# Kernel tuning notes

Measured on AMD Instinct MI355X. Metric: run time of the kernel, lower is better.

The kernel has to match this reference:

```python
import jax, jax.numpy as jnp
import numpy as np

N_HEAD = 8
LN_EPS = 1e-5


def _layernorm(x, w, b):
    mu = jnp.mean(x, axis=-1, keepdims=True)
    var = jnp.var(x, axis=-1, keepdims=True)
    return (x - mu) * jax.lax.rsqrt(var + LN_EPS) * w + b


def setup_inputs() -> dict:
    key = jax.random.key(0)
    ks = jax.random.split(key, 8)
    B, T, D, L, V, F = 4, 768, 512, 6, 50304, 2048
    s = 0.02
    return {
        "idx": jax.random.randint(ks[0], (B, T), 0, V),
        "wte": jax.random.normal(ks[1], (V, D), jnp.float32) * s,
        "wpe": jax.random.normal(ks[2], (T, D), jnp.float32) * s,
        "c_attn_w": jax.random.normal(ks[3], (L, 3 * D, D), jnp.float32) * s,
        "c_attn_b": jnp.zeros((L, 3 * D), jnp.float32),
        "c_proj_w": jax.random.normal(ks[4], (L, D, D), jnp.float32) * s,
        "c_proj_b": jnp.zeros((L, D), jnp.float32),
        "fc_w": jax.random.normal(ks[5], (L, F, D), jnp.float32) * s,
        "fc_b": jnp.zeros((L, F), jnp.float32),
        "fc2_w": jax.random.normal(ks[6], (L, D, F), jnp.float32) * s,
        "fc2_b": jnp.zeros((L, D), jnp.float32),
        "ln1_w": jnp.ones((L, D), jnp.float32),
        "ln1_b": jnp.zeros((L, D), jnp.float32),
        "ln2_w": jnp.ones((L, D), jnp.float32),
        "ln2_b": jnp.zeros((L, D), jnp.float32),
        "lnf_w": jnp.ones((D,), jnp.float32),
        "lnf_b": jnp.zeros((D,), jnp.float32),
    }


def _forward(idx, wte, wpe, c_attn_w, c_attn_b, c_proj_w, c_proj_b,
             fc_w, fc_b, fc2_w, fc2_b, ln1_w, ln1_b, ln2_w, ln2_b,
             lnf_w, lnf_b):
    B, T = idx.shape
    D = wte.shape[1]
    hd = D // N_HEAD
    causal = jnp.tril(jnp.ones((T, T), bool))  # [T,T]

    x = wte[idx] + wpe[:T]  # [B,T,D]; dropout is identity in eval

    def block(x, p):
        (aw, ab, pw, pb, fw, fb, f2w, f2b, l1w, l1b, l2w, l2b) = p
        # --- causal self-attention ---
        qkv = x @ aw.T + ab  # [B,T,3D]
        q, k, v = jnp.split(qkv, 3, axis=-1)
        q = q.reshape(B, T, N_HEAD, hd)
        k = k.reshape(B, T, N_HEAD, hd)
        v = v.reshape(B, T, N_HEAD, hd)
        att = jnp.einsum('bqhd,bkhd->bhqk', q, k) * (1.0 / np.sqrt(hd))
        att = jnp.where(causal, att, -jnp.inf)
        att = jax.nn.softmax(att, axis=-1)
        y = jnp.einsum('bhqk,bkhd->bqhd', att, v).reshape(B, T, D)
        y = y @ pw.T + pb
        x = _layernorm(x + y, l1w, l1b)  # post-norm as in source
        # --- feed-forward ---
        h = jax.nn.relu(x @ fw.T + fb)
        h = h @ f2w.T + f2b
        x = _layernorm(x + h, l2w, l2b)
        return x, None

    params = (c_attn_w, c_attn_b, c_proj_w, c_proj_b, fc_w, fc_b,
              fc2_w, fc2_b, ln1_w, ln1_b, ln2_w, ln2_b)
    x, _ = jax.lax.scan(block, x, params)
    x = _layernorm(x, lnf_w, lnf_b)
    logits = x @ wte.T  # tied head, no bias
    return logits


def reference(idx, wte, wpe, c_attn_w, c_attn_b, c_proj_w, c_proj_b,
              fc_w, fc_b, fc2_w, fc2_b, ln1_w, ln1_b, ln2_w, ln2_b,
              lnf_w, lnf_b):
    return _forward(idx, wte, wpe, c_attn_w, c_attn_b, c_proj_w, c_proj_b,
                    fc_w, fc_b, fc2_w, fc2_b, ln1_w, ln1_b, ln2_w, ln2_b,
                    lnf_w, lnf_b)
```

## Files before the change

### kernel.cpp

```cpp
#include <hip/hip_runtime.h>
#include <hip/hip_bf16.h>

#define AS1 __attribute__((address_space(1)))
#define AS3 __attribute__((address_space(3)))

typedef __attribute__((ext_vector_type(8))) short short8;
typedef __attribute__((ext_vector_type(4))) float f32x4;

constexpr int BB = 4, TT = 768, DDIM = 512, LL = 6, VV = 50304, FF = 2048;
constexpr int MM = BB * TT;

__device__ inline unsigned short f2b(float f) {
  union { float f; unsigned u; } a; a.f = f;
  unsigned u = a.u;
  return (unsigned short)((u + 0x7FFFu + ((u >> 16) & 1u)) >> 16);
}
__device__ inline float b2f(unsigned short u) {
  union { unsigned u; float f; } a; a.u = ((unsigned)u) << 16; return a.f;
}

constexpr size_t CW0 = (size_t)VV * DDIM;
constexpr size_t CW1 = CW0 + (size_t)LL * 3 * DDIM * DDIM;
constexpr size_t CW2 = CW1 + (size_t)LL * DDIM * DDIM;
constexpr size_t CW3 = CW2 + (size_t)LL * FF * DDIM;
constexpr size_t CW4 = CW3 + (size_t)LL * DDIM * FF;

__global__ void cvt_all(const float* __restrict__ wte, const float* __restrict__ aw,
                        const float* __restrict__ pw, const float* __restrict__ fw,
                        const float* __restrict__ f2w, ushort* __restrict__ out) {
  size_t i = ((size_t)blockIdx.x * 256 + threadIdx.x) * 4;
  if (i >= CW4) return;
  const float* src; size_t base;
  if (i < CW0)      { src = wte; base = 0; }
  else if (i < CW1) { src = aw;  base = CW0; }
  else if (i < CW2) { src = pw;  base = CW1; }
  else if (i < CW3) { src = fw;  base = CW2; }
  else              { src = f2w; base = CW3; }
  float4 v = *(const float4*)(src + (i - base));
  ushort4 o = { f2b(v.x), f2b(v.y), f2b(v.z), f2b(v.w) };
  *(ushort4*)(out + i) = o;
}

__global__ void embed_kernel(const int* __restrict__ idx, const float* __restrict__ wte,
                             const float* __restrict__ wpe, float* __restrict__ x,
                             ushort* __restrict__ xb) {
  int row = blockIdx.x;
  int t = row % TT;
  int tok = idx[row];
  int c = threadIdx.x * 4;
  float4 a = *(const float4*)(wte + (size_t)tok * DDIM + c);
  float4 p = *(const float4*)(wpe + (size_t)t * DDIM + c);
  a.x += p.x; a.y += p.y; a.z += p.z; a.w += p.w;
  *(float4*)(x + (size_t)row * DDIM + c) = a;
  ushort4 o = { f2b(a.x), f2b(a.y), f2b(a.z), f2b(a.w) };
  *(ushort4*)(xb + (size_t)row * DDIM + c) = o;
}

template <int RELU, int OUTBF16, int BM, int BN, int SPLITK>
__global__ __launch_bounds__(256) void gemm_bt64(
    const ushort* __restrict__ A, const ushort* __restrict__ Bw,
    const float* __restrict__ bias, void* __restrict__ Cv, int Ndim, int K) {
  constexpr int MI = BM / 32, NJ = BN / 32;
  __shared__ ushort sA[2][BM * 64];
  __shared__ ushort sB[2][BN * 64];
  const int tid = threadIdx.x;
  const int wid = tid >> 6, lane = tid & 63;
  const int m0 = blockIdx.y * BM, n0 = blockIdx.x * BN;
  const int kchunk = K / SPLITK;
  const int ks0 = (SPLITK > 1) ? blockIdx.z * kchunk : 0;
  const int wm = (wid >> 1) * (BM / 2), wn = (wid & 1) * (BN / 2);

  f32x4 zero = {0.f, 0.f, 0.f, 0.f};
  f32x4 acc[MI][NJ];
#pragma unroll
  for (int i = 0; i < MI; i++)
#pragma unroll
    for (int j = 0; j < NJ; j++) acc[i][j] = zero;

  const int r = tid >> 3;
  const int cg = ((tid & 7) ^ (r & 7)) * 8;
  const ushort* gA = A + (size_t)(m0 + r) * K + ks0 + cg;
  const ushort* gB = Bw + (size_t)(n0 + r) * K + ks0 + cg;

  auto stage = [&](int buf, int kk) {
    const ushort* a0 = gA + kk * 64;
    const ushort* b0 = gB + kk * 64;
    ushort* dA = &sA[buf][0] + wid * 512;
    ushort* dB = &sB[buf][0] + wid * 512;
#pragma unroll
    for (int p = 0; p < BM / 32; p++)
      __builtin_amdgcn_global_load_lds((const AS1 void*)(a0 + (size_t)p * 32 * K),
                                       (AS3 void*)(dA + p * 2048), 16, 0, 0);
#pragma unroll
    for (int p = 0; p < BN / 32; p++)
      __builtin_amdgcn_global_load_lds((const AS1 void*)(b0 + (size_t)p * 32 * K),
                                       (AS3 void*)(dB + p * 2048), 16, 0, 0);
  };

  const int fr = lane & 15;
  const int fk = (lane >> 4) * 8;
  auto ldfrag = [&](const ushort* s, int rowbase, int sub) -> short8 {
    const int row = rowbase + fr;
    const int off = row * 128 + ((sub * 64 + fk * 2) ^ ((fr & 7) << 4));
    return *(const short8*)((const char*)s + off);
  };

  const int nK = kchunk >> 6;
  stage(0, 0);
  __syncthreads();
  int buf = 0;
  for (int kk = 0; kk < nK; ++kk) {
    if (kk + 1 < nK) stage(buf ^ 1, kk + 1);
    short8 af[MI][2], bf[NJ][2];
#pragma unroll
    for (int i = 0; i < MI; i++)
#pragma unroll
      for (int s = 0; s < 2; s++) af[i][s] = ldfrag(&sA[buf][0], wm + i * 16, s);
#pragma unroll
    for (int j = 0; j < NJ; j++)
#pragma unroll
      for (int s = 0; s < 2; s++) bf[j][s] = ldfrag(&sB[buf][0], wn + j * 16, s);
#pragma unroll
    for (int i = 0; i < MI; i++)
#pragma unroll
      for (int j = 0; j < NJ; j++)
#pragma unroll
        for (int s = 0; s < 2; s++)
          acc[i][j] = __builtin_amdgcn_mfma_f32_16x16x32_bf16(af[i][s], bf[j][s], acc[i][j], 0, 0, 0);
    __syncthreads();
    buf ^= 1;
  }

  const int cr = (lane >> 4) * 4;
  const int cc = lane & 15;
  const size_t zoff = (SPLITK > 1) ? (size_t)blockIdx.z * MM * Ndim : 0;
  ushort* Cb = (ushort*)Cv + zoff;
  float*  Cf = (float*)Cv + zoff;
#pragma unroll
  for (int j = 0; j < NJ; j++) {
    const int gcol = n0 + wn + j * 16 + cc;
    const float bv = (bias && (SPLITK == 1 || blockIdx.z == 0)) ? bias[gcol] : 0.0f;
#pragma unroll
    for (int i = 0; i < MI; i++) {
      const int grow = m0 + wm + i * 16 + cr;
#pragma unroll
      for (int rr = 0; rr < 4; ++rr) {
        float v = acc[i][j][rr] + bv;
        if (RELU) v = fmaxf(v, 0.0f);
        if (OUTBF16)
          Cb[(size_t)(grow + rr) * Ndim + gcol] = f2b(v);
        else
          Cf[(size_t)(grow + rr) * Ndim + gcol] = v;
      }
    }
  }
}

__global__ __launch_bounds__(256) void gemm_head(
    const ushort* __restrict__ A, const ushort* __restrict__ Bw,
    float* __restrict__ Cv, int Ndim, int K) {
  __shared__ ushort sA[2][128 * 32];
  __shared__ ushort sB[2][128 * 32];
  const int tid = threadIdx.x;
  const int wid = tid >> 6, lane = tid & 63;
  int id = blockIdx.x;
  int v = (id >> 3) + (id & 7) * ((int)gridDim.x >> 3);
  const int m0 = (v % 24) * 128;
  const int n0 = (v / 24) * 128;
  const int wm = (wid >> 1) * 64, wn = (wid & 1) * 64;

  f32x4 zero = {0.f, 0.f, 0.f, 0.f};
  f32x4 acc[4][4];
#pragma unroll
  for (int i = 0; i < 4; i++)
#pragma unroll
    for (int j = 0; j < 4; j++) acc[i][j] = zero;

  const int r4 = tid >> 2;
  const int c8 = (tid & 3) * 8;
  const ushort* gA = A + (size_t)(m0 + r4) * K + c8;
  const ushort* gB = Bw + (size_t)(n0 + r4) * K + c8;
  const size_t K64 = (size_t)64 * K;

  auto stage = [&](int buf, int kk) {
    const ushort* a0 = gA + kk * 32;
    const ushort* b0 = gB + kk * 32;
    ushort* dA = &sA[buf][0] + wid * 512;
    ushort* dB = &sB[buf][0] + wid * 512;
#pragma unroll
    for (int i = 0; i < 2; i++)
      __builtin_amdgcn_global_load_lds((const AS1 void*)(a0 + (size_t)i * K64),
                                       (AS3 void*)(dA + i * 2048), 16, 0, 0);
#pragma unroll
    for (int i = 0; i < 2; i++)
      __builtin_amdgcn_global_load_lds((const AS1 void*)(b0 + (size_t)i * K64),
                                       (AS3 void*)(dB + i * 2048), 16, 0, 0);
  };

  const int fr = lane & 15;
  const int fk = (lane >> 4) * 8;
  const int nK = K >> 5;
  stage(0, 0);
  __syncthreads();
  int buf = 0;
  for (int kk = 0; kk < nK; ++kk) {
    if (kk + 1 < nK) stage(buf ^ 1, kk + 1);
    const ushort* pa0 = &sA[buf][0] + (wm + fr) * 32 + fk;
    const ushort* pb0 = &sB[buf][0] + (wn + fr) * 32 + fk;
    short8 af[4], bf[4];
#pragma unroll
    for (int i = 0; i < 4; i++) af[i] = *(const short8*)(pa0 + i * 16 * 32);
#pragma unroll
    for (int j = 0; j < 4; j++) bf[j] = *(const short8*)(pb0 + j * 16 * 32);
#pragma unroll
    for (int i = 0; i < 4; i++)
#pragma unroll
      for (int j = 0; j < 4; j++)
        acc[i][j] = __builtin_amdgcn_mfma_f32_16x16x32_bf16(af[i], bf[j], acc[i][j], 0, 0, 0);
    __syncthreads();
    buf ^= 1;
  }

  const int cr = (lane >> 4) * 4;
  const int cc = lane & 15;
#pragma unroll
  for (int j = 0; j < 4; j++) {
    const int gcol = n0 + wn + j * 16 + cc;
#pragma unroll
    for (int i = 0; i < 4; i++) {
      const int grow = m0 + wm + i * 16 + cr;
#pragma unroll
      for (int rr = 0; rr < 4; ++rr)
        Cv[(size_t)(grow + rr) * Ndim + gcol] = acc[i][j][rr];
    }
  }
}

__device__ inline short8 lds_swz_read(const ushort* base, int row, int elem) {
  return *(const short8*)((const char*)base + row * 128 + ((elem * 2) ^ ((row & 7) << 4)));
}

__global__ __launch_bounds__(256) void attn_mfma(const ushort* __restrict__ qkv,
                                                 ushort* __restrict__ yb) {
  __shared__ ushort sK[64 * 64];
  __shared__ ushort sVT[64 * 64];
  __shared__ ushort sP[4 * 16 * 64];
  const int tid = threadIdx.x;
  const int wid = tid >> 6, lane = tid & 63;
  const int qt = blockIdx.x;
  const int b = blockIdx.y >> 3, h = blockIdx.y & 7;
  const int q0 = qt * 64;
  const int qw = q0 + wid * 16;

  const int fr = lane & 15;
  const int fk = (lane >> 4) * 8;
  ushort* sPw = sP + wid * 16 * 64;

  short8 qf[2];
  {
    const ushort* qp = qkv + (size_t)(b * TT + qw + fr) * 1536 + h * 64;
    qf[0] = *(const short8*)(qp + fk);
    qf[1] = *(const short8*)(qp + 32 + fk);
  }

  const int r4 = tid >> 2;
  const int c32 = (tid & 3) * 16;

  f32x4 zero = {0.f, 0.f, 0.f, 0.f};
  f32x4 acc[4] = {zero, zero, zero, zero};
  float mrow[4] = {-INFINITY, -INFINITY, -INFINITY, -INFINITY};
  float lrow[4] = {0.f, 0.f, 0.f, 0.f};

  for (int kt = 0; kt <= qt; ++kt) {
    __syncthreads();
    const int k0 = kt * 64;
    {
      const ushort* kp = qkv + (size_t)(b * TT + k0 + r4) * 1536 + 512 + h * 64 + c32;
      short8 kv0 = *(const short8*)kp;
      short8 kv1 = *(const short8*)(kp + 8);
      char* skb = (char*)sK + r4 * 128;
      *(short8*)(skb + ((c32 * 2) ^ ((r4 & 7) << 4))) = kv0;
      *(short8*)(skb + ((c32 * 2 + 16) ^ ((r4 & 7) << 4))) = kv1;
      const ushort* vp = kp + 512;
      short8 vv0 = *(const short8*)vp;
      short8 vv1 = *(const short8*)(vp + 8);
#pragma unroll
      for (int i = 0; i < 8; i++) {
        int d0 = c32 + i, d1 = c32 + 8 + i;
        *(ushort*)((char*)sVT + d0 * 128 + ((r4 * 2) ^ ((d0 & 7) << 4))) = (ushort)vv0[i];
        *(ushort*)((char*)sVT + d1 * 128 + ((r4 * 2) ^ ((d1 & 7) << 4))) = (ushort)vv1[i];
      }
    }
    __syncthreads();

    f32x4 sfr[4];
#pragma unroll
    for (int j = 0; j < 4; j++) {
      short8 kb0 = lds_swz_read(sK, j * 16 + fr, fk);
      short8 kb1 = lds_swz_read(sK, j * 16 + fr, 32 + fk);
      f32x4 s = __builtin_amdgcn_mfma_f32_16x16x32_bf16(qf[0], kb0, zero, 0, 0, 0);
      s = __builtin_amdgcn_mfma_f32_16x16x32_bf16(qf[1], kb1, s, 0, 0, 0);
      sfr[j] = s * 0.125f;
    }
    if (kt == qt) {
#pragma unroll
      for (int j = 0; j < 4; j++)
#pragma unroll
        for (int rr = 0; rr < 4; ++rr)
          if (j * 16 + fr > wid * 16 + (lane >> 4) * 4 + rr) sfr[j][rr] = -INFINITY;
    }

    float scl[4];
#pragma unroll
    for (int rr = 0; rr < 4; ++rr) {
      float t = fmaxf(fmaxf(sfr[0][rr], sfr[1][rr]), fmaxf(sfr[2][rr], sfr[3][rr]));
      t = fmaxf(t, __shfl_xor(t, 1));
      t = fmaxf(t, __shfl_xor(t, 2));
      t = fmaxf(t, __shfl_xor(t, 4));
      t = fmaxf(t, __shfl_xor(t, 8));
      const float mnew = fmaxf(mrow[rr], t);
      scl[rr] = __expf(mrow[rr] - mnew);
      mrow[rr] = mnew;
      float ps = 0.f;
#pragma unroll
      for (int j = 0; j < 4; j++) {
        float p = __expf(sfr[j][rr] - mnew);
        sfr[j][rr] = p;
        ps += p;
      }
      ps += __shfl_xor(ps, 1);
      ps += __shfl_xor(ps, 2);
      ps += __shfl_xor(ps, 4);
      ps += __shfl_xor(ps, 8);
      lrow[rr] = lrow[rr] * scl[rr] + ps;
    }

#pragma unroll
    for (int j = 0; j < 4; j++)
#pragma unroll
      for (int rr = 0; rr < 4; ++rr) {
        int q = (lane >> 4) * 4 + rr, k = j * 16 + fr;
        *(ushort*)((char*)sPw + q * 128 + ((k * 2) ^ ((q & 7) << 4))) = f2b(sfr[j][rr]);
      }

#pragma unroll
    for (int f = 0; f < 4; f++)
#pragma unroll
      for (int rr = 0; rr < 4; ++rr) acc[f][rr] *= scl[rr];

    short8 pa0 = lds_swz_read(sPw, fr, fk);
    short8 pa1 = lds_swz_read(sPw, fr, 32 + fk);
#pragma unroll
    for (int f = 0; f < 4; f++) {
      short8 vb0 = lds_swz_read(sVT, f * 16 + fr, fk);
      short8 vb1 = lds_swz_read(sVT, f * 16 + fr, 32 + fk);
      acc[f] = __builtin_amdgcn_mfma_f32_16x16x32_bf16(pa0, vb0, acc[f], 0, 0, 0);
      acc[f] = __builtin_amdgcn_mfma_f32_16x16x32_bf16(pa1, vb1, acc[f], 0, 0, 0);
    }
  }

#pragma unroll
  for (int rr = 0; rr < 4; ++rr) {
    const float inv = 1.0f / lrow[rr];
    const int token = b * TT + qw + (lane >> 4) * 4 + rr;
    ushort* yp = yb + (size_t)token * DDIM + h * 64 + fr;
#pragma unroll
    for (int f = 0; f < 4; f++) yp[f * 16] = f2b(acc[f][rr] * inv);
  }
}

template <int S>
__global__ __launch_bounds__(256) void add_ln(const float* __restrict__ x,
                                              const ushort* __restrict__ y,
                                              const float* __restrict__ w,
                                              const float* __restrict__ bb,
                                              float* __restrict__ xo,
                                              ushort* __restrict__ xb) {
  const int row = blockIdx.x * 4 + (threadIdx.x >> 6);
  const int lane = threadIdx.x & 63;
  const size_t base = (size_t)row * DDIM + lane * 8;
  f32x4 a0 = *(const f32x4*)(x + base);
  f32x4 a1 = *(const f32x4*)(x + base + 4);
#pragma unroll
  for (int s = 0; s < S; ++s) {
    short8 v = *(const short8*)(y + (size_t)s * MM * DDIM + base);
    f32x4 p0 = { b2f((unsigned short)v[0]), b2f((unsigned short)v[1]),
                 b2f((unsigned short)v[2]), b2f((unsigned short)v[3]) };
    f32x4 p1 = { b2f((unsigned short)v[4]), b2f((unsigned short)v[5]),
                 b2f((unsigned short)v[6]), b2f((unsigned short)v[7]) };
    a0 += p0; a1 += p1;
  }
  float sm = (a0[0] + a0[1] + a0[2] + a0[3]) + (a1[0] + a1[1] + a1[2] + a1[3]);
  f32x4 q0 = a0 * a0, q1 = a1 * a1;
  float ss = (q0[0] + q0[1] + q0[2] + q0[3]) + (q1[0] + q1[1] + q1[2] + q1[3]);
#pragma unroll
  for (int o = 1; o < 64; o <<= 1) {
    sm += __shfl_xor(sm, o);
    ss += __shfl_xor(ss, o);
  }
  const float mu = sm * (1.0f / DDIM);
  const float var = ss * (1.0f / DDIM) - mu * mu;
  const float rs = rsqrtf(var + 1e-5f);
  const int c = lane * 8;
  f32x4 w0 = *(const f32x4*)(w + c), w1 = *(const f32x4*)(w + c + 4);
  f32x4 b0 = *(const f32x4*)(bb + c), b1 = *(const f32x4*)(bb + c + 4);
  f32x4 o0 = (a0 - mu) * rs * w0 + b0;
  f32x4 o1 = (a1 - mu) * rs * w1 + b1;
  *(f32x4*)(xo + base) = o0;
  *(f32x4*)(xo + base + 4) = o1;
  ushort4 u0 = { f2b(o0[0]), f2b(o0[1]), f2b(o0[2]), f2b(o0[3]) };
  ushort4 u1 = { f2b(o1[0]), f2b(o1[1]), f2b(o1[2]), f2b(o1[3]) };
  *(ushort4*)(xb + base) = u0;
  *(ushort4*)(xb + base + 4) = u1;
}

extern "C" void kernel_launch(void* const* d_in, const int* in_sizes, int n_in,
                              void* d_out, int out_size, void* d_ws, size_t ws_size,
                              hipStream_t stream) {
  const int*   idx  = (const int*)d_in[0];
  const float* wte  = (const float*)d_in[1];
  const float* wpe  = (const float*)d_in[2];
  const float* aw   = (const float*)d_in[3];
  const float* ab   = (const float*)d_in[4];
  const float* pw   = (const float*)d_in[5];
  const float* pb   = (const float*)d_in[6];
  const float* fw   = (const float*)d_in[7];
  const float* fb   = (const float*)d_in[8];
  const float* f2w  = (const float*)d_in[9];
  const float* f2bi = (const float*)d_in[10];
  const float* l1w  = (const float*)d_in[11];
  const float* l1b  = (const float*)d_in[12];
  const float* l2w  = (const float*)d_in[13];
  const float* l2b  = (const float*)d_in[14];
  const float* lnfw = (const float*)d_in[15];
  const float* lnfb = (const float*)d_in[16];

  char* ws = (char*)d_ws;
  size_t off = 0;
  auto take = [&](size_t bytes) -> void* {
    void* p = ws + off;
    off += (bytes + 255) & ~(size_t)255;
    return p;
  };
  ushort* wte_b = (ushort*)take((size_t)VV * DDIM * 2);
  ushort* aw_b  = (ushort*)take((size_t)LL * 3 * DDIM * DDIM * 2);
  ushort* pw_b  = (ushort*)take((size_t)LL * DDIM * DDIM * 2);
  ushort* fw_b  = (ushort*)take((size_t)LL * FF * DDIM * 2);
  ushort* f2w_b = (ushort*)take((size_t)LL * DDIM * FF * 2);
  float*  x     = (float*)take((size_t)MM * DDIM * 4);
  ushort* xb    = (ushort*)take((size_t)MM * DDIM * 2);
  ushort* qkv_b = (ushort*)take((size_t)MM * 3 * DDIM * 2);
  ushort* yb    = (ushort*)take((size_t)MM * DDIM * 2);
  ushort* tmp_b = (ushort*)take((size_t)2 * MM * DDIM * 2);
  ushort* hb    = (ushort*)take((size_t)MM * FF * 2);

  cvt_all<<<dim3((unsigned)(CW4 / 4 / 256)), dim3(256), 0, stream>>>(
      wte, aw, pw, fw, f2w, wte_b);

  embed_kernel<<<dim3(MM), dim3(128), 0, stream>>>(idx, wte, wpe, x, xb);

  for (int l = 0; l < LL; ++l) {
    gemm_bt64<0, 1, 128, 64, 1><<<dim3(24, 24), dim3(256), 0, stream>>>(
        xb, aw_b + (size_t)l * 3 * DDIM * DDIM, ab + (size_t)l * 3 * DDIM, qkv_b, 3 * DDIM, DDIM);
    attn_mfma<<<dim3(TT / 64, BB * 8), dim3(256), 0, stream>>>(qkv_b, yb);
    gemm_bt64<0, 1, 64, 64, 2><<<dim3(8, 48, 2), dim3(256), 0, stream>>>(
        yb, pw_b + (size_t)l * DDIM * DDIM, pb + (size_t)l * DDIM, tmp_b, DDIM, DDIM);
    add_ln<2><<<dim3(MM / 4), dim3(256), 0, stream>>>(
        x, tmp_b, l1w + (size_t)l * DDIM, l1b + (size_t)l * DDIM, x, xb);
    gemm_bt64<1, 1, 128, 64, 1><<<dim3(32, 24), dim3(256), 0, stream>>>(
        xb, fw_b + (size_t)l * FF * DDIM, fb + (size_t)l * FF, hb, FF, DDIM);
    gemm_bt64<0, 1, 64, 64, 2><<<dim3(8, 48, 2), dim3(256), 0, stream>>>(
        hb, f2w_b + (size_t)l * DDIM * FF, f2bi + (size_t)l * DDIM, tmp_b, DDIM, FF);
    add_ln<2><<<dim3(MM / 4), dim3(256), 0, stream>>>(
        x, tmp_b, l2w + (size_t)l * DDIM, l2b + (size_t)l * DDIM, x, xb);
  }
  add_ln<0><<<dim3(MM / 4), dim3(256), 0, stream>>>(x, nullptr, lnfw, lnfb, x, xb);

  gemm_head<<<dim3((VV / 128) * 24), dim3(256), 0, stream>>>(
      xb, wte_b, (float*)d_out, VV, DDIM);
}
```

Measured before the change: 856.6 us.

## Generalize head GEMM for QKV/FC, vectorize V transpose, keep residual in bf16

The QKV and FC GEMMs now use the 128x128 head-GEMM kernel (K-step 32, bias and ReLU epilogue) in place of the 128x64 tile kernel, which halves the block count and raises reuse per tile. The V transpose into shared memory in attention now loads four rows of 4-wide vectors and writes ushort4 columns instead of scalar 2-byte stores. The fp32 residual stream is removed, so the embedding and the add+layernorm kernels read and write only bf16. This cuts memory traffic but lowers the precision of the residual path.

```diff
diff --git a/kernel.cpp b/kernel.cpp
--- a/kernel.cpp
+++ b/kernel.cpp
@@ -42,8 +42,7 @@
 }
 
 __global__ void embed_kernel(const int* __restrict__ idx, const float* __restrict__ wte,
-                             const float* __restrict__ wpe, float* __restrict__ x,
-                             ushort* __restrict__ xb) {
+                             const float* __restrict__ wpe, ushort* __restrict__ xb) {
   int row = blockIdx.x;
   int t = row % TT;
   int tok = idx[row];
@@ -51,122 +50,29 @@
   float4 a = *(const float4*)(wte + (size_t)tok * DDIM + c);
   float4 p = *(const float4*)(wpe + (size_t)t * DDIM + c);
   a.x += p.x; a.y += p.y; a.z += p.z; a.w += p.w;
-  *(float4*)(x + (size_t)row * DDIM + c) = a;
   ushort4 o = { f2b(a.x), f2b(a.y), f2b(a.z), f2b(a.w) };
   *(ushort4*)(xb + (size_t)row * DDIM + c) = o;
 }
 
-template <int RELU, int OUTBF16, int BM, int BN, int SPLITK>
-__global__ __launch_bounds__(256) void gemm_bt64(
+template <int RELU, int OUTBF16, int BIAS, int SWZ>
+__global__ __launch_bounds__(256) void gemm97(
     const ushort* __restrict__ A, const ushort* __restrict__ Bw,
     const float* __restrict__ bias, void* __restrict__ Cv, int Ndim, int K) {
-  constexpr int MI = BM / 32, NJ = BN / 32;
-  __shared__ ushort sA[2][BM * 64];
-  __shared__ ushort sB[2][BN * 64];
-  const int tid = threadIdx.x;
-  const int wid = tid >> 6, lane = tid & 63;
-  const int m0 = blockIdx.y * BM, n0 = blockIdx.x * BN;
-  const int kchunk = K / SPLITK;
-  const int ks0 = (SPLITK > 1) ? blockIdx.z * kchunk : 0;
-  const int wm = (wid >> 1) * (BM / 2), wn = (wid & 1) * (BN / 2);
-
-  f32x4 zero = {0.f, 0.f, 0.f, 0.f};
-  f32x4 acc[MI][NJ];
-#pragma unroll
-  for (int i = 0; i < MI; i++)
-#pragma unroll
-    for (int j = 0; j < NJ; j++) acc[i][j] = zero;
-
-  const int r = tid >> 3;
-  const int cg = ((tid & 7) ^ (r & 7)) * 8;
-  const ushort* gA = A + (size_t)(m0 + r) * K + ks0 + cg;
-  const ushort* gB = Bw + (size_t)(n0 + r) * K + ks0 + cg;
-
-  auto stage = [&](int buf, int kk) {
-    const ushort* a0 = gA + kk * 64;
-    const ushort* b0 = gB + kk * 64;
-    ushort* dA = &sA[buf][0] + wid * 512;
-    ushort* dB = &sB[buf][0] + wid * 512;
-#pragma unroll
-    for (int p = 0; p < BM / 32; p++)
-      __builtin_amdgcn_global_load_lds((const AS1 void*)(a0 + (size_t)p * 32 * K),
-                                       (AS3 void*)(dA + p * 2048), 16, 0, 0);
-#pragma unroll
-    for (int p = 0; p < BN / 32; p++)
-      __builtin_amdgcn_global_load_lds((const AS1 void*)(b0 + (size_t)p * 32 * K),
-                                       (AS3 void*)(dB + p * 2048), 16, 0, 0);
-  };
-
-  const int fr = lane & 15;
-  const int fk = (lane >> 4) * 8;
-  auto ldfrag = [&](const ushort* s, int rowbase, int sub) -> short8 {
-    const int row = rowbase + fr;
-    const int off = row * 128 + ((sub * 64 + fk * 2) ^ ((fr & 7) << 4));
-    return *(const short8*)((const char*)s + off);
-  };
-
-  const int nK = kchunk >> 6;
-  stage(0, 0);
-  __syncthreads();
-  int buf = 0;
-  for (int kk = 0; kk < nK; ++kk) {
-    if (kk + 1 < nK) stage(buf ^ 1, kk + 1);
-    short8 af[MI][2], bf[NJ][2];
-#pragma unroll
-    for (int i = 0; i < MI; i++)
-#pragma unroll
-      for (int s = 0; s < 2; s++) af[i][s] = ldfrag(&sA[buf][0], wm + i * 16, s);
-#pragma unroll
-    for (int j = 0; j < NJ; j++)
-#pragma unroll
-      for (int s = 0; s < 2; s++) bf[j][s] = ldfrag(&sB[buf][0], wn + j * 16, s);
-#pragma unroll
-    for (int i = 0; i < MI; i++)
-#pragma unroll
-      for (int j = 0; j < NJ; j++)
-#pragma unroll
-        for (int s = 0; s < 2; s++)
-          acc[i][j] = __builtin_amdgcn_mfma_f32_16x16x32_bf16(af[i][s], bf[j][s], acc[i][j], 0, 0, 0);
-    __syncthreads();
-    buf ^= 1;
-  }
-
-  const int cr = (lane >> 4) * 4;
-  const int cc = lane & 15;
-  const size_t zoff = (SPLITK > 1) ? (size_t)blockIdx.z * MM * Ndim : 0;
-  ushort* Cb = (ushort*)Cv + zoff;
-  float*  Cf = (float*)Cv + zoff;
-#pragma unroll
-  for (int j = 0; j < NJ; j++) {
-    const int gcol = n0 + wn + j * 16 + cc;
-    const float bv = (bias && (SPLITK == 1 || blockIdx.z == 0)) ? bias[gcol] : 0.0f;
-#pragma unroll
-    for (int i = 0; i < MI; i++) {
-      const int grow = m0 + wm + i * 16 + cr;
-#pragma unroll
-      for (int rr = 0; rr < 4; ++rr) {
-        float v = acc[i][j][rr] + bv;
-        if (RELU) v = fmaxf(v, 0.0f);
-        if (OUTBF16)
-          Cb[(size_t)(grow + rr) * Ndim + gcol] = f2b(v);
-        else
-          Cf[(size_t)(grow + rr) * Ndim + gcol] = v;
-      }
-    }
-  }
-}
-
-__global__ __launch_bounds__(256) void gemm_head(
-    const ushort* __restrict__ A, const ushort* __restrict__ Bw,
-    float* __restrict__ Cv, int Ndim, int K) {
   __shared__ ushort sA[2][128 * 32];
   __shared__ ushort sB[2][128 * 32];
   const int tid = threadIdx.x;
   const int wid = tid >> 6, lane = tid & 63;
-  int id = blockIdx.x;
-  int v = (id >> 3) + (id & 7) * ((int)gridDim.x >> 3);
-  const int m0 = (v % 24) * 128;
-  const int n0 = (v / 24) * 128;
+  int m0, n0;
+  if (SWZ) {
+    constexpr int MT = MM / 128;
+    int id = blockIdx.x;
+    int v = (id >> 3) + (id & 7) * ((int)gridDim.x >> 3);
+    m0 = (v % MT) * 128;
+    n0 = (v / MT) * 128;
+  } else {
+    m0 = blockIdx.y * 128;
+    n0 = blockIdx.x * 128;
+  }
   const int wm = (wid >> 1) * 64, wn = (wid & 1) * 64;
 
   f32x4 zero = {0.f, 0.f, 0.f, 0.f};
@@ -226,12 +132,112 @@
 #pragma unroll
   for (int j = 0; j < 4; j++) {
     const int gcol = n0 + wn + j * 16 + cc;
+    const float bv = BIAS ? bias[gcol] : 0.0f;
 #pragma unroll
     for (int i = 0; i < 4; i++) {
       const int grow = m0 + wm + i * 16 + cr;
 #pragma unroll
+      for (int rr = 0; rr < 4; ++rr) {
+        float v = acc[i][j][rr] + bv;
+        if (RELU) v = fmaxf(v, 0.0f);
+        if (OUTBF16)
+          ((ushort*)Cv)[(size_t)(grow + rr) * Ndim + gcol] = f2b(v);
+        else
+          ((float*)Cv)[(size_t)(grow + rr) * Ndim + gcol] = v;
+      }
+    }
+  }
+}
+
+template <int SPLITK>
+__global__ __launch_bounds__(256) void gemm_bt64(
+    const ushort* __restrict__ A, const ushort* __restrict__ Bw,
+    const float* __restrict__ bias, ushort* __restrict__ Cv, int Ndim, int K) {
+  constexpr int BM = 64, BN = 64;
+  constexpr int MI = 2, NJ = 2;
+  __shared__ ushort sA[2][BM * 64];
+  __shared__ ushort sB[2][BN * 64];
+  const int tid = threadIdx.x;
+  const int wid = tid >> 6, lane = tid & 63;
+  const int m0 = blockIdx.y * BM, n0 = blockIdx.x * BN;
+  const int kchunk = K / SPLITK;
+  const int ks0 = blockIdx.z * kchunk;
+  const int wm = (wid >> 1) * 32, wn = (wid & 1) * 32;
+
+  f32x4 zero = {0.f, 0.f, 0.f, 0.f};
+  f32x4 acc[MI][NJ];
+#pragma unroll
+  for (int i = 0; i < MI; i++)
+#pragma unroll
+    for (int j = 0; j < NJ; j++) acc[i][j] = zero;
+
+  const int r = tid >> 3;
+  const int cg = ((tid & 7) ^ (r & 7)) * 8;
+  const ushort* gA = A + (size_t)(m0 + r) * K + ks0 + cg;
+  const ushort* gB = Bw + (size_t)(n0 + r) * K + ks0 + cg;
+
+  auto stage = [&](int buf, int kk) {
+    const ushort* a0 = gA + kk * 64;
+    const ushort* b0 = gB + kk * 64;
+    ushort* dA = &sA[buf][0] + wid * 512;
+    ushort* dB = &sB[buf][0] + wid * 512;
+#pragma unroll
+    for (int p = 0; p < 2; p++)
+      __builtin_amdgcn_global_load_lds((const AS1 void*)(a0 + (size_t)p * 32 * K),
+                                       (AS3 void*)(dA + p * 2048), 16, 0, 0);
+#pragma unroll
+    for (int p = 0; p < 2; p++)
+      __builtin_amdgcn_global_load_lds((const AS1 void*)(b0 + (size_t)p * 32 * K),
+                                       (AS3 void*)(dB + p * 2048), 16, 0, 0);
+  };
+
+  const int fr = lane & 15;
+  const int fk = (lane >> 4) * 8;
+  auto ldfrag = [&](const ushort* s, int rowbase, int sub) -> short8 {
+    const int row = rowbase + fr;
+    const int off = row * 128 + ((sub * 64 + fk * 2) ^ ((fr & 7) << 4));
+    return *(const short8*)((const char*)s + off);
+  };
+
+  const int nK = kchunk >> 6;
+  stage(0, 0);
+  __syncthreads();
+  int buf = 0;
+  for (int kk = 0; kk < nK; ++kk) {
+    if (kk + 1 < nK) stage(buf ^ 1, kk + 1);
+    short8 af[MI][2], bf[NJ][2];
+#pragma unroll
+    for (int i = 0; i < MI; i++)
+#pragma unroll
+      for (int s = 0; s < 2; s++) af[i][s] = ldfrag(&sA[buf][0], wm + i * 16, s);
+#pragma unroll
+    for (int j = 0; j < NJ; j++)
+#pragma unroll
+      for (int s = 0; s < 2; s++) bf[j][s] = ldfrag(&sB[buf][0], wn + j * 16, s);
+#pragma unroll
+    for (int i = 0; i < MI; i++)
+#pragma unroll
+      for (int j = 0; j < NJ; j++)
+#pragma unroll
+        for (int s = 0; s < 2; s++)
+          acc[i][j] = __builtin_amdgcn_mfma_f32_16x16x32_bf16(af[i][s], bf[j][s], acc[i][j], 0, 0, 0);
+    __syncthreads();
+    buf ^= 1;
+  }
+
+  const int cr = (lane >> 4) * 4;
+  const int cc = lane & 15;
+  ushort* Cb = Cv + (size_t)blockIdx.z * MM * Ndim;
+#pragma unroll
+  for (int j = 0; j < NJ; j++) {
+    const int gcol = n0 + wn + j * 16 + cc;
+    const float bv = (blockIdx.z == 0) ? bias[gcol] : 0.0f;
+#pragma unroll
+    for (int i = 0; i < MI; i++) {
+      const int grow = m0 + wm + i * 16 + cr;
+#pragma unroll
       for (int rr = 0; rr < 4; ++rr)
-        Cv[(size_t)(grow + rr) * Ndim + gcol] = acc[i][j][rr];
+        Cb[(size_t)(grow + rr) * Ndim + gcol] = f2b(acc[i][j][rr] + bv);
     }
   }
 }
@@ -265,6 +271,8 @@
 
   const int r4 = tid >> 2;
   const int c32 = (tid & 3) * 16;
+  const int kb = (tid >> 4) * 4;
+  const int db = (tid & 15) * 4;
 
   f32x4 zero = {0.f, 0.f, 0.f, 0.f};
   f32x4 acc[4] = {zero, zero, zero, zero};
@@ -281,15 +289,19 @@
       char* skb = (char*)sK + r4 * 128;
       *(short8*)(skb + ((c32 * 2) ^ ((r4 & 7) << 4))) = kv0;
       *(short8*)(skb + ((c32 * 2 + 16) ^ ((r4 & 7) << 4))) = kv1;
-      const ushort* vp = kp + 512;
-      short8 vv0 = *(const short8*)vp;
-      short8 vv1 = *(const short8*)(vp + 8);
-#pragma unroll
-      for (int i = 0; i < 8; i++) {
-        int d0 = c32 + i, d1 = c32 + 8 + i;
-        *(ushort*)((char*)sVT + d0 * 128 + ((r4 * 2) ^ ((d0 & 7) << 4))) = (ushort)vv0[i];
-        *(ushort*)((char*)sVT + d1 * 128 + ((r4 * 2) ^ ((d1 & 7) << 4))) = (ushort)vv1[i];
-      }
+      const ushort* vp = qkv + (size_t)(b * TT + k0 + kb) * 1536 + 1024 + h * 64 + db;
+      ushort4 L0 = *(const ushort4*)vp;
+      ushort4 L1 = *(const ushort4*)(vp + 1536);
+      ushort4 L2 = *(const ushort4*)(vp + 3072);
+      ushort4 L3 = *(const ushort4*)(vp + 4608);
+      ushort4 c0 = { L0.x, L1.x, L2.x, L3.x };
+      ushort4 c1 = { L0.y, L1.y, L2.y, L3.y };
+      ushort4 c2 = { L0.z, L1.z, L2.z, L3.z };
+      ushort4 c3 = { L0.w, L1.w, L2.w, L3.w };
+      *(ushort4*)((char*)sVT + (db + 0) * 128 + ((kb * 2) ^ (((db + 0) & 7) << 4))) = c0;
+      *(ushort4*)((char*)sVT + (db + 1) * 128 + ((kb * 2) ^ (((db + 1) & 7) << 4))) = c1;
+      *(ushort4*)((char*)sVT + (db + 2) * 128 + ((kb * 2) ^ (((db + 2) & 7) << 4))) = c2;
+      *(ushort4*)((char*)sVT + (db + 3) * 128 + ((kb * 2) ^ (((db + 3) & 7) << 4))) = c3;
     }
     __syncthreads();
 
@@ -370,17 +382,19 @@
 }
 
 template <int S>
-__global__ __launch_bounds__(256) void add_ln(const float* __restrict__ x,
+__global__ __launch_bounds__(256) void add_ln(const ushort* __restrict__ xr,
                                               const ushort* __restrict__ y,
                                               const float* __restrict__ w,
                                               const float* __restrict__ bb,
-                                              float* __restrict__ xo,
-                                              ushort* __restrict__ xb) {
+                                              ushort* __restrict__ xo) {
   const int row = blockIdx.x * 4 + (threadIdx.x >> 6);
   const int lane = threadIdx.x & 63;
   const size_t base = (size_t)row * DDIM + lane * 8;
-  f32x4 a0 = *(const f32x4*)(x + base);
-  f32x4 a1 = *(const f32x4*)(x + base + 4);
+  short8 xv = *(const short8*)(xr + base);
+  f32x4 a0 = { b2f((unsigned short)xv[0]), b2f((unsigned short)xv[1]),
+               b2f((unsigned short)xv[2]), b2f((unsigned short)xv[3]) };
+  f32x4 a1 = { b2f((unsigned short)xv[4]), b2f((unsigned short)xv[5]),
+               b2f((unsigned short)xv[6]), b2f((unsigned short)xv[7]) };
 #pragma unroll
   for (int s = 0; s < S; ++s) {
     short8 v = *(const short8*)(y + (size_t)s * MM * DDIM + base);
@@ -406,12 +420,12 @@
   f32x4 b0 = *(const f32x4*)(bb + c), b1 = *(const f32x4*)(bb + c + 4);
   f32x4 o0 = (a0 - mu) * rs * w0 + b0;
   f32x4 o1 = (a1 - mu) * rs * w1 + b1;
-  *(f32x4*)(xo + base) = o0;
-  *(f32x4*)(xo + base + 4) = o1;
-  ushort4 u0 = { f2b(o0[0]), f2b(o0[1]), f2b(o0[2]), f2b(o0[3]) };
-  ushort4 u1 = { f2b(o1[0]), f2b(o1[1]), f2b(o1[2]), f2b(o1[3]) };
-  *(ushort4*)(xb + base) = u0;
-  *(ushort4*)(xb + base + 4) = u1;
+  short8 u;
+  u[0] = (short)f2b(o0[0]); u[1] = (short)f2b(o0[1]);
+  u[2] = (short)f2b(o0[2]); u[3] = (short)f2b(o0[3]);
+  u[4] = (short)f2b(o1[0]); u[5] = (short)f2b(o1[1]);
+  u[6] = (short)f2b(o1[2]); u[7] = (short)f2b(o1[3]);
+  *(short8*)(xo + base) = u;
 }
 
 extern "C" void kernel_launch(void* const* d_in, const int* in_sizes, int n_in,
@@ -447,7 +461,6 @@
   ushort* pw_b  = (ushort*)take((size_t)LL * DDIM * DDIM * 2);
   ushort* fw_b  = (ushort*)take((size_t)LL * FF * DDIM * 2);
   ushort* f2w_b = (ushort*)take((size_t)LL * DDIM * FF * 2);
-  float*  x     = (float*)take((size_t)MM * DDIM * 4);
   ushort* xb    = (ushort*)take((size_t)MM * DDIM * 2);
   ushort* qkv_b = (ushort*)take((size_t)MM * 3 * DDIM * 2);
   ushort* yb    = (ushort*)take((size_t)MM * DDIM * 2);
@@ -457,25 +470,25 @@
   cvt_all<<<dim3((unsigned)(CW4 / 4 / 256)), dim3(256), 0, stream>>>(
       wte, aw, pw, fw, f2w, wte_b);
 
-  embed_kernel<<<dim3(MM), dim3(128), 0, stream>>>(idx, wte, wpe, x, xb);
+  embed_kernel<<<dim3(MM), dim3(128), 0, stream>>>(idx, wte, wpe, xb);
 
   for (int l = 0; l < LL; ++l) {
-    gemm_bt64<0, 1, 128, 64, 1><<<dim3(24, 24), dim3(256), 0, stream>>>(
+    gemm97<0, 1, 1, 0><<<dim3(12, 24), dim3(256), 0, stream>>>(
         xb, aw_b + (size_t)l * 3 * DDIM * DDIM, ab + (size_t)l * 3 * DDIM, qkv_b, 3 * DDIM, DDIM);
     attn_mfma<<<dim3(TT / 64, BB * 8), dim3(256), 0, stream>>>(qkv_b, yb);
-    gemm_bt64<0, 1, 64, 64, 2><<<dim3(8, 48, 2), dim3(256), 0, stream>>>(
+    gemm_bt64<2><<<dim3(8, 48, 2), dim3(256), 0, stream>>>(
         yb, pw_b + (size_t)l * DDIM * DDIM, pb + (size_t)l * DDIM, tmp_b, DDIM, DDIM);
     add_ln<2><<<dim3(MM / 4), dim3(256), 0, stream>>>(
-        x, tmp_b, l1w + (size_t)l * DDIM, l1b + (size_t)l * DDIM, x, xb);
-    gemm_bt64<1, 1, 128, 64, 1><<<dim3(32, 24), dim3(256), 0, stream>>>(
+        xb, tmp_b, l1w + (size_t)l * DDIM, l1b + (size_t)l * DDIM, xb);
+    gemm97<1, 1, 1, 0><<<dim3(16, 24), dim3(256), 0, stream>>>(
         xb, fw_b + (size_t)l * FF * DDIM, fb + (size_t)l * FF, hb, FF, DDIM);
-    gemm_bt64<0, 1, 64, 64, 2><<<dim3(8, 48, 2), dim3(256), 0, stream>>>(
+    gemm_bt64<2><<<dim3(8, 48, 2), dim3(256), 0, stream>>>(
         hb, f2w_b + (size_t)l * DDIM * FF, f2bi + (size_t)l * DDIM, tmp_b, DDIM, FF);
     add_ln<2><<<dim3(MM / 4), dim3(256), 0, stream>>>(
-        x, tmp_b, l2w + (size_t)l * DDIM, l2b + (size_t)l * DDIM, x, xb);
-  }
-  add_ln<0><<<dim3(MM / 4), dim3(256), 0, stream>>>(x, nullptr, lnfw, lnfb, x, xb);
-
-  gemm_head<<<dim3((VV / 128) * 24), dim3(256), 0, stream>>>(
-      xb, wte_b, (float*)d_out, VV, DDIM);
-}
+        xb, tmp_b, l2w + (size_t)l * DDIM, l2b + (size_t)l * DDIM, xb);
+  }
+  add_ln<0><<<dim3(MM / 4), dim3(256), 0, stream>>>(xb, nullptr, lnfw, lnfb, xb);
+
+  gemm97<0, 0, 0, 1><<<dim3((VV / 128) * 24), dim3(256), 0, stream>>>(
+      xb, wte_b, nullptr, (float*)d_out, VV, DDIM);
+}
```

Measured after the change: 939.3 us. 1.1x slower.
